# Optimization experiments

Hardware: AMD Instinct MI355X
Metric: run time of the kernel (lower is better)

## Reference

```python
import jax, jax.numpy as jnp
import numpy as np

B, S, IN, OUT = 4, 2048, 4096, 1024
ROUNDS = 12  # prime_factors(4096) == [2]*12
QMIN, QMAX = -128, 127


def _create_noise(key, shape, lo, hi):
    # Obfuscation noise spanning the data range; exactly corrected in forward.
    return jax.random.uniform(key, shape, jnp.float32, -0.5, 0.5) * (hi - lo)


def setup_inputs() -> dict:
    key = jax.random.key(0)
    ks = jax.random.split(key, 6)
    x = jax.random.normal(ks[0], (B, S, IN), jnp.float32)
    weight = jax.random.normal(ks[1], (OUT, IN), jnp.float32) * 0.02
    bias = jax.random.normal(ks[2], (OUT,), jnp.float32) * 0.02
    weight_noise = _create_noise(ks[3], (OUT, IN), weight.min(), weight.max())
    noise_x = _create_noise(ks[4], (B, S, IN), x.min(), x.max())
    # one random permutation of in_features per round
    perms = jnp.stack([jax.random.permutation(jax.random.fold_in(key, 1000 + r), IN)
                       for r in range(ROUNDS)]).astype(jnp.int32)
    # 2048 random orthogonal 2x2 blocks per round (rotations, like ortho_group with dim=2)
    theta = jax.random.uniform(ks[5], (ROUNDS, IN // 2), jnp.float32, 0.0, 2.0 * np.pi)
    c, s = jnp.cos(theta), jnp.sin(theta)
    row0 = jnp.stack([c, -s], axis=-1)
    row1 = jnp.stack([s, c], axis=-1)
    matrices = jnp.stack([row0, row1], axis=-2)  # (ROUNDS, IN//2, 2, 2)
    return {"x": x, "weight": weight, "bias": bias, "weight_noise": weight_noise,
            "noise_x": noise_x, "permutations": perms, "matrices": matrices}


def _permute_matrix_operation(X, perms, mats):
    # X: (..., n, cols). Each round: gather rows by permutation, then apply a
    # block-diagonal orthogonal transform (G blocks of size f along the n axis).
    lead = X.shape[:-2]
    n, cols = X.shape[-2], X.shape[-1]
    G, f = mats.shape[1], mats.shape[2]
    for r in range(mats.shape[0]):
        X = jnp.take(X, perms[r], axis=-2)
        Xb = X.reshape(lead + (G, f, cols))
        X = jnp.einsum('gij,...gjc->...gic', mats[r], Xb).reshape(lead + (n, cols))
    return X


def _quant_dequant(t):
    # Asymmetric per-tensor quantize -> round -> clamp -> dequantize (int8-style).
    lo, hi = t.min(), t.max()
    scale = (hi - lo) / (QMAX - QMIN)
    zp = jnp.round(QMIN - lo / scale)
    q = jnp.clip(jnp.round(t / scale + zp), QMIN, QMAX)
    return (q - zp) * scale


def reference(x, weight, bias, weight_noise, noise_x, permutations, matrices):
    # inverse-transpose blocks; equals `matrices` for orthogonal blocks, kept explicit for fidelity
    inv_mats_mT = jnp.swapaxes(jnp.linalg.inv(matrices), -1, -2)
    w_plus = weight + weight_noise                                   # (OUT, IN)
    permuted_w = jnp.swapaxes(
        _permute_matrix_operation(jnp.swapaxes(w_plus, -1, -2), permutations, inv_mats_mT), -1, -2)
    qw = _quant_dequant(permuted_w)                                  # (OUT, IN)
    permuted_x = jnp.swapaxes(
        _permute_matrix_operation(jnp.swapaxes(x + noise_x, -1, -2), permutations, matrices), -1, -2)
    qx = _quant_dequant(permuted_x)                                  # (B, S, IN)
    res = qx @ qw.T + bias                                           # quantized matmul + bias
    res = res - x @ weight_noise.T                                   # correction term 1
    res = res - noise_x @ w_plus.T                                   # correction term 2
    return res
```

## Files before the change

kernel.cpp:

```cpp
#include <hip/hip_runtime.h>


#define IN_F   4096
#define OUT_F  1024
#define MROWS  8192
#define KTOT   12288
#define NROUNDS 12
#define NPASS  6

typedef _Float16 f16;
typedef _Float16 f16x8 __attribute__((ext_vector_type(8)));
typedef _Float16 f16x4 __attribute__((ext_vector_type(4)));
typedef float    f32x4 __attribute__((ext_vector_type(4)));

#define OFF_XT  (0ull)
#define OFF_WT  (OFF_XT + (size_t)MROWS * IN_F * 4)
#define OFF_A   (OFF_WT + (size_t)OUT_F * IN_F * 4)
#define OFF_B   (OFF_A + (size_t)MROWS * KTOT * 2)
#define OFF_MM  (OFF_B + (size_t)OUT_F * KTOT * 2)
#define OFF_TIX (OFF_MM + 256)
#define OFF_TCX (OFF_TIX + (size_t)NPASS * 2048 * 16)
#define OFF_TIW (OFF_TCX + (size_t)NPASS * 2048 * 32)
#define OFF_TCW (OFF_TIW + (size_t)NPASS * 2048 * 16)

__device__ __forceinline__ unsigned enc_f(float f) {
  unsigned u = __float_as_uint(f);
  return (u & 0x80000000u) ? ~u : (u | 0x80000000u);
}
__device__ __forceinline__ float dec_f(unsigned u) {
  unsigned b = (u & 0x80000000u) ? (u & 0x7fffffffu) : ~u;
  return __uint_as_float(b);
}

__global__ void init_mm_kernel(unsigned* mm) {
  mm[0] = 0xFFFFFFFFu;
  mm[1] = 0u;
  mm[2] = 0xFFFFFFFFu;
  mm[3] = 0u;
}

__global__ void build_tables_kernel(const int* __restrict__ perms,
                                    const float* __restrict__ mats,
                                    int4* __restrict__ tIx, float4* __restrict__ tCx,
                                    int4* __restrict__ tIw, float4* __restrict__ tCw) {
  int p = blockIdx.x;
  int r0 = 2 * p, r1 = 2 * p + 1;
  for (int g = threadIdx.x; g < 2048; g += blockDim.x) {
    int q0 = perms[r1 * IN_F + 2 * g], q1 = perms[r1 * IN_F + 2 * g + 1];
    int a0 = q0 >> 1, e0 = q0 & 1, a1 = q1 >> 1, e1 = q1 & 1;
    int4 idx = make_int4(perms[r0 * IN_F + 2 * a0], perms[r0 * IN_F + 2 * a0 + 1],
                         perms[r0 * IN_F + 2 * a1], perms[r0 * IN_F + 2 * a1 + 1]);
    const float* Ma = mats + ((size_t)r0 * 2048 + a0) * 4;
    const float* Mb = mats + ((size_t)r0 * 2048 + a1) * 4;
    const float* M1 = mats + ((size_t)r1 * 2048 + g) * 4;
    int o = p * 2048 + g;
    {
      float c00 = Ma[e0 * 2], c01 = Ma[e0 * 2 + 1];
      float c10 = Mb[e1 * 2], c11 = Mb[e1 * 2 + 1];
      float m00 = M1[0], m01 = M1[1], m10 = M1[2], m11 = M1[3];
      tIx[o] = idx;
      tCx[2 * o]     = make_float4(m00 * c00, m00 * c01, m01 * c10, m01 * c11);
      tCx[2 * o + 1] = make_float4(m10 * c00, m10 * c01, m11 * c10, m11 * c11);
    }
    {
      float rda = 1.0f / (Ma[0] * Ma[3] - Ma[1] * Ma[2]);
      float rdb = 1.0f / (Mb[0] * Mb[3] - Mb[1] * Mb[2]);
      float rd1 = 1.0f / (M1[0] * M1[3] - M1[1] * M1[2]);
      float c00 = (e0 == 0 ? Ma[3] : -Ma[1]) * rda;
      float c01 = (e0 == 0 ? -Ma[2] : Ma[0]) * rda;
      float c10 = (e1 == 0 ? Mb[3] : -Mb[1]) * rdb;
      float c11 = (e1 == 0 ? -Mb[2] : Mb[0]) * rdb;
      float m00 = M1[3] * rd1, m01 = -M1[2] * rd1;
      float m10 = -M1[1] * rd1, m11 = M1[0] * rd1;
      tIw[o] = idx;
      tCw[2 * o]     = make_float4(m00 * c00, m00 * c01, m01 * c10, m01 * c11);
      tCw[2 * o + 1] = make_float4(m10 * c00, m10 * c01, m11 * c10, m11 * c11);
    }
  }
}

template <bool IS_W>
__global__ __launch_bounds__(256) void transform_kernel(
    const float* __restrict__ in0, const float* __restrict__ in1,
    const int4* __restrict__ tI, const float4* __restrict__ tC,
    float* __restrict__ tout, f16* __restrict__ f16out,
    unsigned* __restrict__ mm, int mmidx) {
  __shared__ float2 buf[2][IN_F];
  const int t = threadIdx.x;
  const size_t m0 = (size_t)blockIdx.x * 2;

  const float4* r0a = (const float4*)(in0 + m0 * IN_F);
  const float4* r0b = (const float4*)(in1 + m0 * IN_F);
  const float4* r1a = (const float4*)(in0 + (m0 + 1) * IN_F);
  const float4* r1b = (const float4*)(in1 + (m0 + 1) * IN_F);
  f16* f0 = f16out + m0 * KTOT;
  f16* f1 = f16out + (m0 + 1) * KTOT;

#pragma unroll
  for (int j = 0; j < 4; j++) {
    int i4 = j * 256 + t;
    float4 a0 = r0a[i4], b0 = r0b[i4], a1 = r1a[i4], b1 = r1b[i4];
    float4 s0 = make_float4(a0.x + b0.x, a0.y + b0.y, a0.z + b0.z, a0.w + b0.w);
    float4 s1 = make_float4(a1.x + b1.x, a1.y + b1.y, a1.z + b1.z, a1.w + b1.w);
    int c = i4 * 4;
    *(float4*)&buf[0][c]     = make_float4(s0.x, s1.x, s0.y, s1.y);
    *(float4*)&buf[0][c + 2] = make_float4(s0.z, s1.z, s0.w, s1.w);
    f16x4 p0, p1, q0, q1;
    if (IS_W) {
      p0.x=(f16)b0.x; p0.y=(f16)b0.y; p0.z=(f16)b0.z; p0.w=(f16)b0.w;
      q0.x=(f16)s0.x; q0.y=(f16)s0.y; q0.z=(f16)s0.z; q0.w=(f16)s0.w;
      p1.x=(f16)b1.x; p1.y=(f16)b1.y; p1.z=(f16)b1.z; p1.w=(f16)b1.w;
      q1.x=(f16)s1.x; q1.y=(f16)s1.y; q1.z=(f16)s1.z; q1.w=(f16)s1.w;
    } else {
      p0.x=(f16)(-a0.x); p0.y=(f16)(-a0.y); p0.z=(f16)(-a0.z); p0.w=(f16)(-a0.w);
      q0.x=(f16)(-b0.x); q0.y=(f16)(-b0.y); q0.z=(f16)(-b0.z); q0.w=(f16)(-b0.w);
      p1.x=(f16)(-a1.x); p1.y=(f16)(-a1.y); p1.z=(f16)(-a1.z); p1.w=(f16)(-a1.w);
      q1.x=(f16)(-b1.x); q1.y=(f16)(-b1.y); q1.z=(f16)(-b1.z); q1.w=(f16)(-b1.w);
    }
    *(f16x4*)(f0 + IN_F + c)     = p0;
    *(f16x4*)(f0 + 2 * IN_F + c) = q0;
    *(f16x4*)(f1 + IN_F + c)     = p1;
    *(f16x4*)(f1 + 2 * IN_F + c) = q1;
  }
  __syncthreads();

  int cur = 0;
  for (int pass = 0; pass < NPASS; pass++) {
    const int4* ti = tI + pass * 2048;
    const float4* tc = tC + (size_t)pass * 4096;
#pragma unroll
    for (int i = 0; i < 8; i++) {
      int g = i * 256 + t;
      int4 id = ti[g];
      float4 cA = tc[2 * g], cB = tc[2 * g + 1];
      float2 x0 = buf[cur][id.x], x1 = buf[cur][id.y];
      float2 x2 = buf[cur][id.z], x3 = buf[cur][id.w];
      float y0x = cA.x * x0.x + cA.y * x1.x + cA.z * x2.x + cA.w * x3.x;
      float y0y = cA.x * x0.y + cA.y * x1.y + cA.z * x2.y + cA.w * x3.y;
      float y1x = cB.x * x0.x + cB.y * x1.x + cB.z * x2.x + cB.w * x3.x;
      float y1y = cB.x * x0.y + cB.y * x1.y + cB.z * x2.y + cB.w * x3.y;
      *(float4*)&buf[cur ^ 1][2 * g] = make_float4(y0x, y0y, y1x, y1y);
    }
    cur ^= 1;
    __syncthreads();
  }
  float lmin = 3.4e38f, lmax = -3.4e38f;
  float4* o0 = (float4*)(tout + m0 * IN_F);
  float4* o1 = (float4*)(tout + (m0 + 1) * IN_F);
#pragma unroll
  for (int j = 0; j < 4; j++) {
    int i4 = j * 256 + t;
    int c = i4 * 4;
    float4 q0 = *(float4*)&buf[0][c];
    float4 q1 = *(float4*)&buf[0][c + 2];
    o0[i4] = make_float4(q0.x, q0.z, q1.x, q1.z);
    o1[i4] = make_float4(q0.y, q0.w, q1.y, q1.w);
    lmin = fminf(lmin, fminf(fminf(q0.x, q0.y), fminf(q0.z, q0.w)));
    lmin = fminf(lmin, fminf(fminf(q1.x, q1.y), fminf(q1.z, q1.w)));
    lmax = fmaxf(lmax, fmaxf(fmaxf(q0.x, q0.y), fmaxf(q0.z, q0.w)));
    lmax = fmaxf(lmax, fmaxf(fmaxf(q1.x, q1.y), fmaxf(q1.z, q1.w)));
  }
#pragma unroll
  for (int off = 32; off > 0; off >>= 1) {
    lmin = fminf(lmin, __shfl_down(lmin, off));
    lmax = fmaxf(lmax, __shfl_down(lmax, off));
  }
  float* red = (float*)&buf[1][0];
  int wid = t >> 6;
  if ((t & 63) == 0) { red[wid * 2] = lmin; red[wid * 2 + 1] = lmax; }
  __syncthreads();
  if (t == 0) {
    float bmin = fminf(fminf(red[0], red[2]), fminf(red[4], red[6]));
    float bmax = fmaxf(fmaxf(red[1], red[3]), fmaxf(red[5], red[7]));
    atomicMin(&mm[mmidx], enc_f(bmin));
    atomicMax(&mm[mmidx + 1], enc_f(bmax));
  }
}

__global__ void finalize_kernel(unsigned* mm) {
  float* sc = (float*)(mm + 4);
  float xlo = dec_f(mm[0]), xhi = dec_f(mm[1]);
  float wlo = dec_f(mm[2]), whi = dec_f(mm[3]);
  float sx = (xhi - xlo) / 255.0f;
  float zx = rintf(-128.0f - xlo / sx);
  float sw = (whi - wlo) / 255.0f;
  float zw = rintf(-128.0f - wlo / sw);
  sc[0] = sx; sc[1] = zx; sc[2] = sw; sc[3] = zw;
}

__global__ __launch_bounds__(256) void quant_kernel(
    const float* __restrict__ src, f16* __restrict__ dst,
    const unsigned* __restrict__ mm, int scoff) {
  const float* sc = (const float*)(mm + 4);
  float s = sc[scoff], zp = sc[scoff + 1];
  int m = blockIdx.x, t = threadIdx.x;
  const float4* srow = (const float4*)(src + (size_t)m * IN_F);
  f16* drow = dst + (size_t)m * KTOT;
#pragma unroll
  for (int j = 0; j < 4; j++) {
    int i4 = j * 256 + t;
    float4 v = srow[i4];
    float q0 = (fminf(fmaxf(rintf(v.x / s + zp), -128.f), 127.f) - zp) * s;
    float q1 = (fminf(fmaxf(rintf(v.y / s + zp), -128.f), 127.f) - zp) * s;
    float q2 = (fminf(fmaxf(rintf(v.z / s + zp), -128.f), 127.f) - zp) * s;
    float q3 = (fminf(fmaxf(rintf(v.w / s + zp), -128.f), 127.f) - zp) * s;
    f16x4 o; o.x = (f16)q0; o.y = (f16)q1; o.z = (f16)q2; o.w = (f16)q3;
    *(f16x4*)(drow + i4 * 4) = o;
  }
}

__device__ __forceinline__ void gl2lds16(const void* g, void* l) {
  __builtin_amdgcn_global_load_lds(
      (__attribute__((address_space(1))) void*)g,
      (__attribute__((address_space(3))) void*)l, 16, 0, 0);
}

__global__ __launch_bounds__(256, 2) void gemm_kernel(
    const f16* __restrict__ A, const f16* __restrict__ B,
    const float* __restrict__ bias, float* __restrict__ out) {
  __shared__ f16 As[128 * 32];
  __shared__ f16 Bs[128 * 32];
  const int tid = threadIdx.x;
  const int wave = tid >> 6, lane = tid & 63;
  const int quad = lane >> 4, fr = lane & 15;
  const int bm = blockIdx.x & 63, bn = blockIdx.x >> 6;
  const int wm = (wave & 1) * 64, wn = (wave >> 1) * 64;

  f32x4 acc[4][4] = {};

  const int l4 = lane >> 2;
  const int lc = (lane & 3) * 8;
  const size_t arow = (size_t)(bm * 128 + wave * 16 + l4);
  const size_t brow = (size_t)(bn * 128 + wave * 16 + l4);
  const f16* ag0 = A + arow * KTOT + lc;
  const f16* ag1 = A + (arow + 64) * KTOT + lc;
  const f16* bg0 = B + brow * KTOT + lc;
  const f16* bg1 = B + (brow + 64) * KTOT + lc;
  f16* as0 = As + (wave * 16) * 32;
  f16* as1 = As + (64 + wave * 16) * 32;
  f16* bs0 = Bs + (wave * 16) * 32;
  f16* bs1 = Bs + (64 + wave * 16) * 32;

  for (int kk = 0; kk < KTOT; kk += 32) {
    gl2lds16(ag0 + kk, as0);
    gl2lds16(ag1 + kk, as1);
    gl2lds16(bg0 + kk, bs0);
    gl2lds16(bg1 + kk, bs1);
    __syncthreads();
    f16x8 af[4], bf[4];
#pragma unroll
    for (int mi = 0; mi < 4; mi++)
      af[mi] = *(const f16x8*)(As + (wm + mi * 16 + fr) * 32 + quad * 8);
#pragma unroll
    for (int ni = 0; ni < 4; ni++)
      bf[ni] = *(const f16x8*)(Bs + (wn + ni * 16 + fr) * 32 + quad * 8);
#pragma unroll
    for (int mi = 0; mi < 4; mi++)
#pragma unroll
      for (int ni = 0; ni < 4; ni++)
        acc[mi][ni] = __builtin_amdgcn_mfma_f32_16x16x32_f16(
            af[mi], bf[ni], acc[mi][ni], 0, 0, 0);
    __syncthreads();
  }

#pragma unroll
  for (int mi = 0; mi < 4; mi++) {
    int gm = bm * 128 + wm + mi * 16 + quad * 4;
#pragma unroll
    for (int ni = 0; ni < 4; ni++) {
      int gn = bn * 128 + wn + ni * 16 + fr;
      float bv = bias[gn];
#pragma unroll
      for (int e = 0; e < 4; e++)
        out[(size_t)(gm + e) * OUT_F + gn] = acc[mi][ni][e] + bv;
    }
  }
}

extern "C" void kernel_launch(void* const* d_in, const int* in_sizes, int n_in,
                              void* d_out, int out_size, void* d_ws, size_t ws_size,
                              hipStream_t stream) {
  const float* x     = (const float*)d_in[0];
  const float* w     = (const float*)d_in[1];
  const float* bias  = (const float*)d_in[2];
  const float* wn    = (const float*)d_in[3];
  const float* nx    = (const float*)d_in[4];
  const int*   perms = (const int*)d_in[5];
  const float* mats  = (const float*)d_in[6];
  float* out = (float*)d_out;

  char* ws = (char*)d_ws;
  float* xt   = (float*)(ws + OFF_XT);
  float* wt   = (float*)(ws + OFF_WT);
  f16*   Aall = (f16*)(ws + OFF_A);
  f16*   Ball = (f16*)(ws + OFF_B);
  unsigned* mm = (unsigned*)(ws + OFF_MM);
  int4*   tIx = (int4*)(ws + OFF_TIX);
  float4* tCx = (float4*)(ws + OFF_TCX);
  int4*   tIw = (int4*)(ws + OFF_TIW);
  float4* tCw = (float4*)(ws + OFF_TCW);

  init_mm_kernel<<<1, 1, 0, stream>>>(mm);
  build_tables_kernel<<<NPASS, 256, 0, stream>>>(perms, mats, tIx, tCx, tIw, tCw);
  transform_kernel<false><<<MROWS / 2, 256, 0, stream>>>(x, nx, tIx, tCx, xt, Aall, mm, 0);
  transform_kernel<true><<<OUT_F / 2, 256, 0, stream>>>(w, wn, tIw, tCw, wt, Ball, mm, 2);
  finalize_kernel<<<1, 1, 0, stream>>>(mm);
  quant_kernel<<<MROWS, 256, 0, stream>>>(xt, Aall, mm, 0);
  quant_kernel<<<OUT_F, 256, 0, stream>>>(wt, Ball, mm, 2);
  gemm_kernel<<<(MROWS / 128) * (OUT_F / 128), 256, 0, stream>>>(Aall, Ball, bias, out);
}
```

Measured before the change: 755.4 us.

## Split-K GEMM with atomics, merge transform and quant launches, pack table indices

The GEMM now splits K into two halves, doubling the grid to 1024 blocks, and accumulates into an output pre-filled with bias using float atomic adds. The x and w transform kernels are merged into one launch of 1024-thread blocks, and the two quant launches are merged into one. Permutation indices are packed as 16-bit pairs to halve table reads, and the min/max init moves into the table-build kernel. The changes target under-occupancy of the 512-block GEMM and launch overhead, at the cost of an extra full output write plus atomic read-modify-write traffic, and run-to-run variation in summation order.

```diff
diff --git a/kernel.cpp b/kernel.cpp
--- a/kernel.cpp
+++ b/kernel.cpp
@@ -5,7 +5,7 @@
 #define OUT_F  1024
 #define MROWS  8192
 #define KTOT   12288
-#define NROUNDS 12
+#define KHALF  6144
 #define NPASS  6
 
 typedef _Float16 f16;
@@ -19,9 +19,9 @@
 #define OFF_B   (OFF_A + (size_t)MROWS * KTOT * 2)
 #define OFF_MM  (OFF_B + (size_t)OUT_F * KTOT * 2)
 #define OFF_TIX (OFF_MM + 256)
-#define OFF_TCX (OFF_TIX + (size_t)NPASS * 2048 * 16)
+#define OFF_TCX (OFF_TIX + (size_t)NPASS * 2048 * 8)
 #define OFF_TIW (OFF_TCX + (size_t)NPASS * 2048 * 32)
-#define OFF_TCW (OFF_TIW + (size_t)NPASS * 2048 * 16)
+#define OFF_TCW (OFF_TIW + (size_t)NPASS * 2048 * 8)
 
 __device__ __forceinline__ unsigned enc_f(float f) {
   unsigned u = __float_as_uint(f);
@@ -32,24 +32,22 @@
   return __uint_as_float(b);
 }
 
-__global__ void init_mm_kernel(unsigned* mm) {
-  mm[0] = 0xFFFFFFFFu;
-  mm[1] = 0u;
-  mm[2] = 0xFFFFFFFFu;
-  mm[3] = 0u;
-}
-
 __global__ void build_tables_kernel(const int* __restrict__ perms,
                                     const float* __restrict__ mats,
-                                    int4* __restrict__ tIx, float4* __restrict__ tCx,
-                                    int4* __restrict__ tIw, float4* __restrict__ tCw) {
+                                    uint2* __restrict__ tIx, float4* __restrict__ tCx,
+                                    uint2* __restrict__ tIw, float4* __restrict__ tCw,
+                                    unsigned* __restrict__ mm) {
+  if (blockIdx.x == 0 && threadIdx.x == 0) {
+    mm[0] = 0xFFFFFFFFu; mm[1] = 0u; mm[2] = 0xFFFFFFFFu; mm[3] = 0u;
+  }
   int p = blockIdx.x;
   int r0 = 2 * p, r1 = 2 * p + 1;
   for (int g = threadIdx.x; g < 2048; g += blockDim.x) {
     int q0 = perms[r1 * IN_F + 2 * g], q1 = perms[r1 * IN_F + 2 * g + 1];
     int a0 = q0 >> 1, e0 = q0 & 1, a1 = q1 >> 1, e1 = q1 & 1;
-    int4 idx = make_int4(perms[r0 * IN_F + 2 * a0], perms[r0 * IN_F + 2 * a0 + 1],
-                         perms[r0 * IN_F + 2 * a1], perms[r0 * IN_F + 2 * a1 + 1]);
+    unsigned i0 = perms[r0 * IN_F + 2 * a0], i1 = perms[r0 * IN_F + 2 * a0 + 1];
+    unsigned i2 = perms[r0 * IN_F + 2 * a1], i3 = perms[r0 * IN_F + 2 * a1 + 1];
+    uint2 idx = make_uint2(i0 | (i1 << 16), i2 | (i3 << 16));
     const float* Ma = mats + ((size_t)r0 * 2048 + a0) * 4;
     const float* Mb = mats + ((size_t)r0 * 2048 + a1) * 4;
     const float* M1 = mats + ((size_t)r1 * 2048 + g) * 4;
@@ -79,34 +77,41 @@
   }
 }
 
-template <bool IS_W>
-__global__ __launch_bounds__(256) void transform_kernel(
-    const float* __restrict__ in0, const float* __restrict__ in1,
-    const int4* __restrict__ tI, const float4* __restrict__ tC,
-    float* __restrict__ tout, f16* __restrict__ f16out,
-    unsigned* __restrict__ mm, int mmidx) {
+__global__ __launch_bounds__(1024) void transform_kernel(
+    const float* __restrict__ x, const float* __restrict__ nx,
+    const float* __restrict__ w, const float* __restrict__ wn,
+    const uint2* __restrict__ tIx, const float4* __restrict__ tCx,
+    const uint2* __restrict__ tIw, const float4* __restrict__ tCw,
+    float* __restrict__ xt, float* __restrict__ wt,
+    f16* __restrict__ Aall, f16* __restrict__ Ball,
+    unsigned* __restrict__ mm) {
   __shared__ float2 buf[2][IN_F];
   const int t = threadIdx.x;
-  const size_t m0 = (size_t)blockIdx.x * 2;
-
-  const float4* r0a = (const float4*)(in0 + m0 * IN_F);
-  const float4* r0b = (const float4*)(in1 + m0 * IN_F);
-  const float4* r1a = (const float4*)(in0 + (m0 + 1) * IN_F);
-  const float4* r1b = (const float4*)(in1 + (m0 + 1) * IN_F);
-  f16* f0 = f16out + m0 * KTOT;
-  f16* f1 = f16out + (m0 + 1) * KTOT;
-
-#pragma unroll
-  for (int j = 0; j < 4; j++) {
-    int i4 = j * 256 + t;
-    float4 a0 = r0a[i4], b0 = r0b[i4], a1 = r1a[i4], b1 = r1b[i4];
+  const bool isW = blockIdx.x >= (MROWS / 2);
+  const float *in0, *in1; const uint2* tI; const float4* tC;
+  float* tout; f16* fout; int mmidx; size_t m0;
+  if (!isW) {
+    m0 = (size_t)blockIdx.x * 2;
+    in0 = x; in1 = nx; tI = tIx; tC = tCx; tout = xt; fout = Aall; mmidx = 0;
+  } else {
+    m0 = (size_t)(blockIdx.x - MROWS / 2) * 2;
+    in0 = w; in1 = wn; tI = tIw; tC = tCw; tout = wt; fout = Ball; mmidx = 2;
+  }
+  f16* f0 = fout + m0 * KTOT;
+  f16* f1 = fout + (m0 + 1) * KTOT;
+
+  {
+    float4 a0 = ((const float4*)(in0 + m0 * IN_F))[t];
+    float4 b0 = ((const float4*)(in1 + m0 * IN_F))[t];
+    float4 a1 = ((const float4*)(in0 + (m0 + 1) * IN_F))[t];
+    float4 b1 = ((const float4*)(in1 + (m0 + 1) * IN_F))[t];
     float4 s0 = make_float4(a0.x + b0.x, a0.y + b0.y, a0.z + b0.z, a0.w + b0.w);
     float4 s1 = make_float4(a1.x + b1.x, a1.y + b1.y, a1.z + b1.z, a1.w + b1.w);
-    int c = i4 * 4;
+    int c = t * 4;
     *(float4*)&buf[0][c]     = make_float4(s0.x, s1.x, s0.y, s1.y);
     *(float4*)&buf[0][c + 2] = make_float4(s0.z, s1.z, s0.w, s1.w);
     f16x4 p0, p1, q0, q1;
-    if (IS_W) {
+    if (isW) {
       p0.x=(f16)b0.x; p0.y=(f16)b0.y; p0.z=(f16)b0.z; p0.w=(f16)b0.w;
       q0.x=(f16)s0.x; q0.y=(f16)s0.y; q0.z=(f16)s0.z; q0.w=(f16)s0.w;
       p1.x=(f16)b1.x; p1.y=(f16)b1.y; p1.z=(f16)b1.z; p1.w=(f16)b1.w;
@@ -126,15 +131,15 @@
 
   int cur = 0;
   for (int pass = 0; pass < NPASS; pass++) {
-    const int4* ti = tI + pass * 2048;
+    const uint2* ti = tI + pass * 2048;
     const float4* tc = tC + (size_t)pass * 4096;
 #pragma unroll
-    for (int i = 0; i < 8; i++) {
-      int g = i * 256 + t;
-      int4 id = ti[g];
+    for (int i = 0; i < 2; i++) {
+      int g = i * 1024 + t;
+      uint2 pk = ti[g];
       float4 cA = tc[2 * g], cB = tc[2 * g + 1];
-      float2 x0 = buf[cur][id.x], x1 = buf[cur][id.y];
-      float2 x2 = buf[cur][id.z], x3 = buf[cur][id.w];
+      float2 x0 = buf[cur][pk.x & 0xffff], x1 = buf[cur][pk.x >> 16];
+      float2 x2 = buf[cur][pk.y & 0xffff], x3 = buf[cur][pk.y >> 16];
       float y0x = cA.x * x0.x + cA.y * x1.x + cA.z * x2.x + cA.w * x3.x;
       float y0y = cA.x * x0.y + cA.y * x1.y + cA.z * x2.y + cA.w * x3.y;
       float y1x = cB.x * x0.x + cB.y * x1.x + cB.z * x2.x + cB.w * x3.x;
@@ -145,20 +150,16 @@
     __syncthreads();
   }
   float lmin = 3.4e38f, lmax = -3.4e38f;
-  float4* o0 = (float4*)(tout + m0 * IN_F);
-  float4* o1 = (float4*)(tout + (m0 + 1) * IN_F);
-#pragma unroll
-  for (int j = 0; j < 4; j++) {
-    int i4 = j * 256 + t;
-    int c = i4 * 4;
+  {
+    int c = t * 4;
     float4 q0 = *(float4*)&buf[0][c];
     float4 q1 = *(float4*)&buf[0][c + 2];
-    o0[i4] = make_float4(q0.x, q0.z, q1.x, q1.z);
-    o1[i4] = make_float4(q0.y, q0.w, q1.y, q1.w);
-    lmin = fminf(lmin, fminf(fminf(q0.x, q0.y), fminf(q0.z, q0.w)));
-    lmin = fminf(lmin, fminf(fminf(q1.x, q1.y), fminf(q1.z, q1.w)));
-    lmax = fmaxf(lmax, fmaxf(fmaxf(q0.x, q0.y), fmaxf(q0.z, q0.w)));
-    lmax = fmaxf(lmax, fmaxf(fmaxf(q1.x, q1.y), fmaxf(q1.z, q1.w)));
+    ((float4*)(tout + m0 * IN_F))[t]       = make_float4(q0.x, q0.z, q1.x, q1.z);
+    ((float4*)(tout + (m0 + 1) * IN_F))[t] = make_float4(q0.y, q0.w, q1.y, q1.w);
+    lmin = fminf(fminf(fminf(q0.x, q0.y), fminf(q0.z, q0.w)),
+                 fminf(fminf(q1.x, q1.y), fminf(q1.z, q1.w)));
+    lmax = fmaxf(fmaxf(fmaxf(q0.x, q0.y), fmaxf(q0.z, q0.w)),
+                 fmaxf(fmaxf(q1.x, q1.y), fmaxf(q1.z, q1.w)));
   }
 #pragma unroll
   for (int off = 32; off > 0; off >>= 1) {
@@ -170,8 +171,12 @@
   if ((t & 63) == 0) { red[wid * 2] = lmin; red[wid * 2 + 1] = lmax; }
   __syncthreads();
   if (t == 0) {
-    float bmin = fminf(fminf(red[0], red[2]), fminf(red[4], red[6]));
-    float bmax = fmaxf(fmaxf(red[1], red[3]), fmaxf(red[5], red[7]));
+    float bmin = red[0], bmax = red[1];
+#pragma unroll
+    for (int i = 1; i < 16; i++) {
+      bmin = fminf(bmin, red[i * 2]);
+      bmax = fmaxf(bmax, red[i * 2 + 1]);
+    }
     atomicMin(&mm[mmidx], enc_f(bmin));
     atomicMax(&mm[mmidx + 1], enc_f(bmax));
   }
@@ -189,13 +194,16 @@
 }
 
 __global__ __launch_bounds__(256) void quant_kernel(
-    const float* __restrict__ src, f16* __restrict__ dst,
-    const unsigned* __restrict__ mm, int scoff) {
+    const float* __restrict__ xt, const float* __restrict__ wt,
+    f16* __restrict__ Aall, f16* __restrict__ Ball,
+    const unsigned* __restrict__ mm) {
   const float* sc = (const float*)(mm + 4);
-  float s = sc[scoff], zp = sc[scoff + 1];
-  int m = blockIdx.x, t = threadIdx.x;
-  const float4* srow = (const float4*)(src + (size_t)m * IN_F);
-  f16* drow = dst + (size_t)m * KTOT;
+  const bool isW = blockIdx.x >= MROWS;
+  int m = isW ? blockIdx.x - MROWS : blockIdx.x;
+  float s = isW ? sc[2] : sc[0], zp = isW ? sc[3] : sc[1];
+  const float4* srow = (const float4*)((isW ? wt : xt) + (size_t)m * IN_F);
+  f16* drow = (isW ? Ball : Aall) + (size_t)m * KTOT;
+  int t = threadIdx.x;
 #pragma unroll
   for (int j = 0; j < 4; j++) {
     int i4 = j * 256 + t;
@@ -209,21 +217,34 @@
   }
 }
 
+__global__ __launch_bounds__(256) void bias_init_kernel(
+    const float* __restrict__ bias, float* __restrict__ out) {
+  const float4* b4 = (const float4*)bias;
+  float4* o4 = (float4*)out;
+  int idx = blockIdx.x * 256 + threadIdx.x;
+  const int total = MROWS * OUT_F / 4;
+  for (int i = idx; i < total; i += gridDim.x * 256)
+    o4[i] = b4[i & (OUT_F / 4 - 1)];
+}
+
 __device__ __forceinline__ void gl2lds16(const void* g, void* l) {
   __builtin_amdgcn_global_load_lds(
       (__attribute__((address_space(1))) void*)g,
       (__attribute__((address_space(3))) void*)l, 16, 0, 0);
 }
 
-__global__ __launch_bounds__(256, 2) void gemm_kernel(
+__global__ __launch_bounds__(256, 4) void gemm_kernel(
     const f16* __restrict__ A, const f16* __restrict__ B,
-    const float* __restrict__ bias, float* __restrict__ out) {
+    float* __restrict__ out) {
   __shared__ f16 As[128 * 32];
   __shared__ f16 Bs[128 * 32];
   const int tid = threadIdx.x;
   const int wave = tid >> 6, lane = tid & 63;
   const int quad = lane >> 4, fr = lane & 15;
-  const int bm = blockIdx.x & 63, bn = blockIdx.x >> 6;
+  const int bm = blockIdx.x & 63;
+  const int bn = (blockIdx.x >> 6) & 7;
+  const int ks = blockIdx.x >> 9;
+  const int k0 = ks * KHALF;
   const int wm = (wave & 1) * 64, wn = (wave >> 1) * 64;
 
   f32x4 acc[4][4] = {};
@@ -232,16 +253,16 @@
   const int lc = (lane & 3) * 8;
   const size_t arow = (size_t)(bm * 128 + wave * 16 + l4);
   const size_t brow = (size_t)(bn * 128 + wave * 16 + l4);
-  const f16* ag0 = A + arow * KTOT + lc;
-  const f16* ag1 = A + (arow + 64) * KTOT + lc;
-  const f16* bg0 = B + brow * KTOT + lc;
-  const f16* bg1 = B + (brow + 64) * KTOT + lc;
+  const f16* ag0 = A + arow * KTOT + k0 + lc;
+  const f16* ag1 = A + (arow + 64) * KTOT + k0 + lc;
+  const f16* bg0 = B + brow * KTOT + k0 + lc;
+  const f16* bg1 = B + (brow + 64) * KTOT + k0 + lc;
   f16* as0 = As + (wave * 16) * 32;
   f16* as1 = As + (64 + wave * 16) * 32;
   f16* bs0 = Bs + (wave * 16) * 32;
   f16* bs1 = Bs + (64 + wave * 16) * 32;
 
-  for (int kk = 0; kk < KTOT; kk += 32) {
+  for (int kk = 0; kk < KHALF; kk += 32) {
     gl2lds16(ag0 + kk, as0);
     gl2lds16(ag1 + kk, as1);
     gl2lds16(bg0 + kk, bs0);
@@ -269,10 +290,9 @@
 #pragma unroll
     for (int ni = 0; ni < 4; ni++) {
       int gn = bn * 128 + wn + ni * 16 + fr;
-      float bv = bias[gn];
 #pragma unroll
       for (int e = 0; e < 4; e++)
-        out[(size_t)(gm + e) * OUT_F + gn] = acc[mi][ni][e] + bv;
+        unsafeAtomicAdd(&out[(size_t)(gm + e) * OUT_F + gn], acc[mi][ni][e]);
     }
   }
 }
@@ -295,17 +315,16 @@
   f16*   Aall = (f16*)(ws + OFF_A);
   f16*   Ball = (f16*)(ws + OFF_B);
   unsigned* mm = (unsigned*)(ws + OFF_MM);
-  int4*   tIx = (int4*)(ws + OFF_TIX);
+  uint2*  tIx = (uint2*)(ws + OFF_TIX);
   float4* tCx = (float4*)(ws + OFF_TCX);
-  int4*   tIw = (int4*)(ws + OFF_TIW);
+  uint2*  tIw = (uint2*)(ws + OFF_TIW);
   float4* tCw = (float4*)(ws + OFF_TCW);
 
-  init_mm_kernel<<<1, 1, 0, stream>>>(mm);
-  build_tables_kernel<<<NPASS, 256, 0, stream>>>(perms, mats, tIx, tCx, tIw, tCw);
-  transform_kernel<false><<<MROWS / 2, 256, 0, stream>>>(x, nx, tIx, tCx, xt, Aall, mm, 0);
-  transform_kernel<true><<<OUT_F / 2, 256, 0, stream>>>(w, wn, tIw, tCw, wt, Ball, mm, 2);
+  build_tables_kernel<<<NPASS, 256, 0, stream>>>(perms, mats, tIx, tCx, tIw, tCw, mm);
+  transform_kernel<<<MROWS / 2 + OUT_F / 2, 1024, 0, stream>>>(
+      x, nx, w, wn, tIx, tCx, tIw, tCw, xt, wt, Aall, Ball, mm);
   finalize_kernel<<<1, 1, 0, stream>>>(mm);
-  quant_kernel<<<MROWS, 256, 0, stream>>>(xt, Aall, mm, 0);
-  quant_kernel<<<OUT_F, 256, 0, stream>>>(wt, Ball, mm, 2);
-  gemm_kernel<<<(MROWS / 128) * (OUT_F / 128), 256, 0, stream>>>(Aall, Ball, bias, out);
-}
+  quant_kernel<<<MROWS + OUT_F, 256, 0, stream>>>(xt, wt, Aall, Ball, mm);
+  bias_init_kernel<<<1024, 256, 0, stream>>>(bias, out);
+  gemm_kernel<<<2 * (MROWS / 128) * (OUT_F / 128), 256, 0, stream>>>(Aall, Ball, out);
+}
```

Result: faster. 736.1 us (-2.6%).
